# Performance work log

Measured on AMD Instinct MI355X. Metric: run time of the kernel, lower is better.

The kernel has to match this reference:

```python
import jax, jax.numpy as jnp
import numpy as np
import math

D_MODEL = 512
N_HEADS = 8
KSIZE = 3
SEQ = 2048
BATCH = 4


def setup_inputs() -> dict:
    key = jax.random.key(0)
    ks = jax.random.split(key, 12)
    f32 = jnp.float32
    scale_in = 1.0 / math.sqrt(D_MODEL)
    inp = {
        "query": jax.random.normal(ks[0], (SEQ, BATCH, D_MODEL), f32),
        "key": jax.random.normal(ks[1], (SEQ, BATCH, D_MODEL), f32),
        "value": jax.random.normal(ks[2], (SEQ, BATCH, D_MODEL), f32),
        # causal mask: 1 where attention allowed (lower triangular), 0 elsewhere
        "attn_mask": jnp.tril(jnp.ones((SEQ, SEQ), jnp.int32)),
        "conv1_w": jax.random.normal(ks[3], (D_MODEL, D_MODEL, KSIZE), f32) * scale_in,
        "conv1_b": jax.random.normal(ks[4], (D_MODEL,), f32) * 0.01,
        "conv2_w": jax.random.normal(ks[5], (D_MODEL, D_MODEL, KSIZE), f32) * scale_in,
        "conv2_b": jax.random.normal(ks[6], (D_MODEL,), f32) * 0.01,
        "lin1_w": jax.random.normal(ks[7], (D_MODEL, D_MODEL), f32) * scale_in,
        "lin1_b": jax.random.normal(ks[8], (D_MODEL,), f32) * 0.01,
        "lin2_w": jax.random.normal(ks[9], (D_MODEL, D_MODEL), f32) * scale_in,
        "lin2_b": jax.random.normal(ks[10], (D_MODEL,), f32) * 0.01,
    }
    return inp


def _causal_conv1d(x, w, b):
    # x: [B, S, C_in]; w: [C_out, C_in, K] (torch Conv1d layout); left-pad K-1 (causal)
    K = w.shape[-1]
    xc = jnp.transpose(x, (0, 2, 1))  # [B, C, S]
    y = jax.lax.conv_general_dilated(
        xc, w, window_strides=(1,), padding=[(K - 1, 0)],
        dimension_numbers=("NCH", "OIH", "NCH"))
    y = y + b[None, :, None]
    return jnp.transpose(y, (0, 2, 1))  # [B, S, C_out]


def reference(query, key, value, attn_mask,
              conv1_w, conv1_b, conv2_w, conv2_b,
              lin1_w, lin1_b, lin2_w, lin2_b):
    h, dk = N_HEADS, D_MODEL // N_HEADS
    S, B, D = query.shape
    q = jnp.transpose(query, (1, 0, 2))  # [B, S, D]
    k = jnp.transpose(key, (1, 0, 2))
    v = jnp.transpose(value, (1, 0, 2))

    q = _causal_conv1d(q, conv1_w, conv1_b).reshape(B, S, h, dk).transpose(0, 2, 1, 3)
    k = _causal_conv1d(k, conv2_w, conv2_b).reshape(B, S, h, dk).transpose(0, 2, 1, 3)
    v = (v @ lin1_w.T + lin1_b).reshape(B, S, h, dk).transpose(0, 2, 1, 3)

    scores = jnp.einsum("bhqd,bhkd->bhqk", q, k) / math.sqrt(dk)
    scores = jnp.where(attn_mask[None, None, :, :] == 0, jnp.float32(-1e9), scores)
    p_attn = jax.nn.softmax(scores, axis=-1)  # dropout p=0.0 (deterministic)
    x = jnp.einsum("bhqk,bhkd->bhqd", p_attn, v)
    x = x.transpose(0, 2, 1, 3).reshape(B, S, D)
    out = x @ lin2_w.T + lin2_b
    return jnp.transpose(out, (1, 0, 2))  # back to [S, B, D]
```

## Files before the change

kernel.cpp:

```cpp
#include <hip/hip_runtime.h>
#include <hip/hip_bf16.h>

#define S_LEN 2048
#define BATCH 4
#define DMODEL 512
#define NHEADS 8
#define DK 64
#define NELEM 4194304
#define WSLOT 786432

typedef __hip_bfloat16 bf16;
typedef unsigned short u16_t;
typedef __attribute__((ext_vector_type(8))) short bfx8;
typedef __attribute__((ext_vector_type(4))) short bfx4;
typedef __attribute__((ext_vector_type(4))) float fx4;

#define MFMA16(a, b, c) __builtin_amdgcn_mfma_f32_16x16x32_bf16(a, b, c, 0, 0, 0)

__device__ __forceinline__ float cvt(float x) { return x; }
__device__ __forceinline__ float cvt(bf16 x) { return __bfloat162float(x); }
__device__ __forceinline__ u16_t f2b(float x) { bf16 h = __float2bfloat16(x); return *(u16_t*)&h; }
__device__ __forceinline__ float b2f16(u16_t u) { bf16 h = *(bf16*)&u; return __bfloat162float(h); }

__global__ void sniff_kernel(const u16_t* __restrict__ q, int* __restrict__ flag) {
    const int lane = threadIdx.x & 63;
    int cnt = 0;
    for (int j = 0; j < 4; j++) {
        int e = (q[2 * (lane + 64 * j)] >> 7) & 0xFF;
        cnt += (int)__popcll(__ballot(e >= 100 && e <= 140));
    }
    if (lane == 0 && blockIdx.x == 0) *flag = (cnt >= 200) ? 1 : 0;
}

__global__ void cvt_in_kernel(const void* __restrict__ q, const void* __restrict__ k,
                              const void* __restrict__ v, u16_t* __restrict__ am,
                              const int* __restrict__ flag) {
    int gid = blockIdx.x * 256 + threadIdx.x;
    int e8 = gid * 8;
    int z = e8 >> 22;
    int off = e8 & (NELEM - 1);
    const void* src = (z == 0) ? q : (z == 1) ? k : v;
    u16_t* dst = am + (size_t)z * NELEM + off;
    if (*flag) {
        *(bfx8*)dst = *(const bfx8*)((const u16_t*)src + off);
    } else {
        const float* s = (const float*)src + off;
        fx4 a = *(const fx4*)s;
        fx4 b = *(const fx4*)(s + 4);
        u16_t tmp[8];
#pragma unroll
        for (int j = 0; j < 4; j++) { tmp[j] = f2b(a[j]); tmp[4 + j] = f2b(b[j]); }
        *(bfx8*)dst = *(const bfx8*)tmp;
    }
}

__global__ void cvt_w_kernel(const void* __restrict__ c1w, const void* __restrict__ c2w,
                             const void* __restrict__ l1w, const void* __restrict__ l2w,
                             const void* __restrict__ b0, const void* __restrict__ b1,
                             const void* __restrict__ b2, const void* __restrict__ b3,
                             u16_t* __restrict__ wt, u16_t* __restrict__ bb,
                             const int* __restrict__ flag) {
    const int isbf = *flag;
    if (blockIdx.x >= 3072) {
        int i = (blockIdx.x - 3072) * 256 + threadIdx.x;
        int p = i >> 9, o = i & 511;
        const void* b = (p == 0) ? b0 : (p == 1) ? b1 : (p == 2) ? b2 : b3;
        bb[i] = f2b(isbf ? cvt(((const bf16*)b)[o]) : ((const float*)b)[o]);
        return;
    }
    int gid = blockIdx.x * 256 + threadIdx.x;
    int e4 = gid * 4;
    int p = e4 / WSLOT;
    int r = e4 - p * WSLOT;
    int t = r >> 18;
    int rem = r & 262143;
    int o = rem >> 9, kk = rem & 511;
    const void* w = (p == 0) ? c1w : (p == 1) ? c2w : (p == 2) ? l1w : l2w;
    u16_t out[4];
#pragma unroll
    for (int j = 0; j < 4; j++) {
        float val;
        if (p < 2) {
            int idx = (o * DMODEL + kk + j) * 3 + t;
            val = isbf ? cvt(((const bf16*)w)[idx]) : ((const float*)w)[idx];
        } else {
            if (t == 2) {
                int idx = o * DMODEL + kk + j;
                val = isbf ? cvt(((const bf16*)w)[idx]) : ((const float*)w)[idx];
            } else val = 0.f;
        }
        out[j] = f2b(val);
    }
    *(bfx4*)(wt + e4) = *(const bfx4*)out;
}

template <int MODE>
__global__ __launch_bounds__(256) void uproj_kernel(
    const u16_t* __restrict__ X, const u16_t* __restrict__ Wt,
    const u16_t* __restrict__ Bb, u16_t* __restrict__ Y,
    void* __restrict__ dout, const int* __restrict__ flag) {
    constexpr int SMEM = (MODE == 0) ? 32832 : 23040;
    __shared__ __align__(16) u16_t smem[SMEM];
    const int tid = threadIdx.x;
    const int wave = tid >> 6, lane = tid & 63;
    const int l16 = lane & 15, quad = lane >> 4;
    const int mb_base = blockIdx.x * 256;
    const int nb_base = blockIdx.y * 64;
    const int z = blockIdx.z;
    const int isconv = (MODE == 0) && (z < 2);
    const u16_t* Xz = X + (size_t)((MODE == 0) ? z : 0) * NELEM;
    const u16_t* Wz = Wt + (size_t)((MODE == 0) ? z : 3) * WSLOT;
    const u16_t* Bz = Bb + ((MODE == 0) ? z : 3) * DMODEL;

    fx4 acc[4][4];
#pragma unroll
    for (int mb = 0; mb < 4; mb++)
#pragma unroll
        for (int nb = 0; nb < 4; nb++) acc[mb][nb] = (fx4){0.f, 0.f, 0.f, 0.f};

    if (isconv) {
        u16_t (*as_)[72] = (u16_t (*)[72])smem;
        u16_t (*ws_)[64][72] = (u16_t (*)[64][72])(smem + 19008);
        bfx8 pa[9], pw[6];
        {
            const int kc = 0;
#pragma unroll
            for (int j = 0; j < 9; j++) {
                int i = tid + 256 * j;
                if (i < 2112) {
                    int r = i >> 3, c8 = (i & 7) << 3;
                    int gm = mb_base - 8 + r;
                    if (gm >= 0) pa[j] = *(const bfx8*)(Xz + (size_t)gm * DMODEL + (kc << 6) + c8);
                    else { bfx8 zv; for (int jj = 0; jj < 8; jj++) zv[jj] = 0; pa[j] = zv; }
                }
            }
#pragma unroll
            for (int j = 0; j < 6; j++) {
                int i = tid + 256 * j;
                int t = i >> 9, rr = (i >> 3) & 63, c8 = (i & 7) << 3;
                pw[j] = *(const bfx8*)(Wz + (size_t)(t * DMODEL + nb_base + rr) * DMODEL + (kc << 6) + c8);
            }
        }
        for (int kc = 0; kc < 8; kc++) {
            __syncthreads();
#pragma unroll
            for (int j = 0; j < 9; j++) {
                int i = tid + 256 * j;
                if (i < 2112) { int r = i >> 3, c8 = (i & 7) << 3; *(bfx8*)&as_[r][c8] = pa[j]; }
            }
#pragma unroll
            for (int j = 0; j < 6; j++) {
                int i = tid + 256 * j;
                int t = i >> 9, rr = (i >> 3) & 63, c8 = (i & 7) << 3;
                *(bfx8*)&ws_[t][rr][c8] = pw[j];
            }
            __syncthreads();
            if (kc < 7) {
                const int kn = kc + 1;
#pragma unroll
                for (int j = 0; j < 9; j++) {
                    int i = tid + 256 * j;
                    if (i < 2112) {
                        int r = i >> 3, c8 = (i & 7) << 3;
                        int gm = mb_base - 8 + r;
                        if (gm >= 0) pa[j] = *(const bfx8*)(Xz + (size_t)gm * DMODEL + (kn << 6) + c8);
                        else { bfx8 zv; for (int jj = 0; jj < 8; jj++) zv[jj] = 0; pa[j] = zv; }
                    }
                }
#pragma unroll
                for (int j = 0; j < 6; j++) {
                    int i = tid + 256 * j;
                    int t = i >> 9, rr = (i >> 3) & 63, c8 = (i & 7) << 3;
                    pw[j] = *(const bfx8*)(Wz + (size_t)(t * DMODEL + nb_base + rr) * DMODEL + (kn << 6) + c8);
                }
            }
#pragma unroll
            for (int c = 0; c < 2; c++) {
#pragma unroll
                for (int t = 0; t < 3; t++) {
                    const int roff = 4 * t;
                    bfx8 av[4];
#pragma unroll
                    for (int mb = 0; mb < 4; mb++)
                        av[mb] = *(const bfx8*)&as_[wave * 64 + mb * 16 + l16 + roff][c * 32 + quad * 8];
#pragma unroll
                    for (int nb = 0; nb < 4; nb++) {
                        bfx8 bfr = *(const bfx8*)&ws_[t][nb * 16 + l16][c * 32 + quad * 8];
#pragma unroll
                        for (int mb = 0; mb < 4; mb++)
                            acc[mb][nb] = MFMA16(av[mb], bfr, acc[mb][nb]);
                    }
                }
            }
        }
    } else {
        u16_t (*as_)[72] = (u16_t (*)[72])smem;
        u16_t (*wsl)[72] = (u16_t (*)[72])(smem + ((MODE == 0) ? 19008 : 18432));
        const u16_t* Wlin = Wz + 2 * (size_t)DMODEL * DMODEL;
        bfx8 pa[8], pw[2];
        {
            const int kc = 0;
#pragma unroll
            for (int j = 0; j < 8; j++) {
                int i = tid + 256 * j;
                int r = i >> 3, c8 = (i & 7) << 3;
                pa[j] = *(const bfx8*)(Xz + (size_t)(mb_base + r) * DMODEL + (kc << 6) + c8);
            }
#pragma unroll
            for (int j = 0; j < 2; j++) {
                int i = tid + 256 * j;
                int rr = i >> 3, c8 = (i & 7) << 3;
                pw[j] = *(const bfx8*)(Wlin + (size_t)(nb_base + rr) * DMODEL + (kc << 6) + c8);
            }
        }
        for (int kc = 0; kc < 8; kc++) {
            __syncthreads();
#pragma unroll
            for (int j = 0; j < 8; j++) {
                int i = tid + 256 * j;
                int r = i >> 3, c8 = (i & 7) << 3;
                *(bfx8*)&as_[r][c8] = pa[j];
            }
#pragma unroll
            for (int j = 0; j < 2; j++) {
                int i = tid + 256 * j;
                int rr = i >> 3, c8 = (i & 7) << 3;
                *(bfx8*)&wsl[rr][c8] = pw[j];
            }
            __syncthreads();
            if (kc < 7) {
                const int kn = kc + 1;
#pragma unroll
                for (int j = 0; j < 8; j++) {
                    int i = tid + 256 * j;
                    int r = i >> 3, c8 = (i & 7) << 3;
                    pa[j] = *(const bfx8*)(Xz + (size_t)(mb_base + r) * DMODEL + (kn << 6) + c8);
                }
#pragma unroll
                for (int j = 0; j < 2; j++) {
                    int i = tid + 256 * j;
                    int rr = i >> 3, c8 = (i & 7) << 3;
                    pw[j] = *(const bfx8*)(Wlin + (size_t)(nb_base + rr) * DMODEL + (kn << 6) + c8);
                }
            }
#pragma unroll
            for (int c = 0; c < 2; c++) {
                bfx8 av[4];
#pragma unroll
                for (int mb = 0; mb < 4; mb++)
                    av[mb] = *(const bfx8*)&as_[wave * 64 + mb * 16 + l16][c * 32 + quad * 8];
#pragma unroll
                for (int nb = 0; nb < 4; nb++) {
                    bfx8 bfr = *(const bfx8*)&wsl[nb * 16 + l16][c * 32 + quad * 8];
#pragma unroll
                    for (int mb = 0; mb < 4; mb++)
                        acc[mb][nb] = MFMA16(av[mb], bfr, acc[mb][nb]);
                }
            }
        }
    }

    const int isbf = *flag;
#pragma unroll
    for (int mb = 0; mb < 4; mb++)
#pragma unroll
        for (int nb = 0; nb < 4; nb++)
#pragma unroll
            for (int r = 0; r < 4; r++) {
                int m = mb_base + wave * 64 + mb * 16 + quad * 4 + r;
                int o = nb_base + nb * 16 + l16;
                float val = acc[mb][nb][r] + b2f16(Bz[o]);
                if (MODE == 0) {
                    int s = m >> 2, b2 = m & 3, h2 = o >> 6, d2 = o & 63;
                    size_t idx = (z == 2)
                        ? (((size_t)(b2 * NHEADS + h2) * DK + d2) * S_LEN + s)
                        : (((size_t)(b2 * NHEADS + h2) * S_LEN + s) * DK + d2);
                    Y[(size_t)z * NELEM + idx] = f2b(val);
                } else {
                    if (isbf) ((bf16*)dout)[(size_t)m * DMODEL + o] = __float2bfloat16(val);
                    else      ((float*)dout)[(size_t)m * DMODEL + o] = val;
                }
            }
}

__global__ __launch_bounds__(256) void mattn_kernel(
    const u16_t* __restrict__ Qp, const u16_t* __restrict__ Kp,
    const u16_t* __restrict__ VpT, u16_t* __restrict__ Out) {
    __shared__ __align__(16) u16_t ks_[64][72];
    __shared__ __align__(16) u16_t vs[64][72];
    const int tid = threadIdx.x, wave = tid >> 6, lane = tid & 63;
    const int l16 = lane & 15, quad = lane >> 4;
    const int flat = (int)blockIdx.y * 16 + (int)blockIdx.x;
    const int swz = (flat & 7) * 64 + (flat >> 3);
    const int bh = swz >> 4;
    const int bx = swz & 15;
    const int bb2 = bh >> 3, hh2 = bh & 7;
    const int qts[2] = {bx, 31 - bx};

    const int r0 = tid >> 3, c8 = (tid & 7) << 3;
    const int pc0 = (c8 & 35) | ((c8 & 16) >> 2) | ((c8 & 12) << 1);
    const int c84 = c8 + 4;
    const int pc1 = (c84 & 35) | ((c84 & 16) >> 2) | ((c84 & 12) << 1);

    bfx8 qa[2][2];
#pragma unroll
    for (int j = 0; j < 2; j++) {
        const u16_t* qptr = Qp + (size_t)(bh * S_LEN + (qts[j] << 6) + wave * 16 + l16) * DK + quad * 8;
        qa[j][0] = *(const bfx8*)qptr;
        qa[j][1] = *(const bfx8*)(qptr + 32);
    }
    fx4 o_[2][4];
    float psum[2] = {0.f, 0.f};
#pragma unroll
    for (int j = 0; j < 2; j++)
#pragma unroll
        for (int nf = 0; nf < 4; nf++) o_[j][nf] = (fx4){0.f, 0.f, 0.f, 0.f};

    bfx8 kf0 = *(const bfx8*)(Kp + (size_t)(bh * S_LEN + r0) * DK + c8);
    bfx8 kf1 = *(const bfx8*)(Kp + (size_t)(bh * S_LEN + r0 + 32) * DK + c8);
    bfx8 vf0 = *(const bfx8*)(VpT + (size_t)(bh * DK + r0) * S_LEN + c8);
    bfx8 vf1 = *(const bfx8*)(VpT + (size_t)(bh * DK + r0 + 32) * S_LEN + c8);

    const int qg0 = (qts[0] << 6) + wave * 16 + l16;
    const int qg1 = (qts[1] << 6) + wave * 16 + l16;

    const int ktmax = qts[1];
    for (int kt = 0; kt <= ktmax; kt++) {
        const int kbase = kt << 6;
        __syncthreads();
        *(bfx8*)&ks_[r0][c8] = kf0;
        *(bfx8*)&ks_[r0 + 32][c8] = kf1;
        {
            bfx4 a0 = {vf0[0], vf0[1], vf0[2], vf0[3]};
            bfx4 a1 = {vf0[4], vf0[5], vf0[6], vf0[7]};
            bfx4 b0 = {vf1[0], vf1[1], vf1[2], vf1[3]};
            bfx4 b1 = {vf1[4], vf1[5], vf1[6], vf1[7]};
            *(bfx4*)&vs[r0][pc0] = a0;
            *(bfx4*)&vs[r0][pc1] = a1;
            *(bfx4*)&vs[r0 + 32][pc0] = b0;
            *(bfx4*)&vs[r0 + 32][pc1] = b1;
        }
        __syncthreads();
        if (kt < ktmax) {
            const int nb = (kt + 1) << 6;
            kf0 = *(const bfx8*)(Kp + (size_t)(bh * S_LEN + nb + r0) * DK + c8);
            kf1 = *(const bfx8*)(Kp + (size_t)(bh * S_LEN + nb + r0 + 32) * DK + c8);
            vf0 = *(const bfx8*)(VpT + (size_t)(bh * DK + r0) * S_LEN + nb + c8);
            vf1 = *(const bfx8*)(VpT + (size_t)(bh * DK + r0 + 32) * S_LEN + nb + c8);
        }

        bfx8 ak[2][4];
#pragma unroll
        for (int c = 0; c < 2; c++)
#pragma unroll
            for (int nf = 0; nf < 4; nf++)
                ak[c][nf] = *(const bfx8*)&ks_[nf * 16 + l16][c * 32 + quad * 8];

        bfx8 pb[2][2];
#pragma unroll
        for (int j = 0; j < 2; j++) {
            if (kt > qts[j]) continue;
            fx4 s[4];
#pragma unroll
            for (int nf = 0; nf < 4; nf++) {
                fx4 a = (fx4){0.f, 0.f, 0.f, 0.f};
                a = MFMA16(ak[0][nf], qa[j][0], a);
                a = MFMA16(ak[1][nf], qa[j][1], a);
                s[nf] = a;
            }
            const bool last = (kt == qts[j]);
            const int qgj = (j == 0) ? qg0 : qg1;
            float tsum = 0.f;
#pragma unroll
            for (int nf = 0; nf < 4; nf++) {
                float pr[4];
#pragma unroll
                for (int r = 0; r < 4; r++) {
                    float p = __builtin_amdgcn_exp2f(fmaf(s[nf][r], 0.18033688f, -17.3123405f));
                    if (last) {
                        int kg = kbase + nf * 16 + quad * 4 + r;
                        if (kg > qgj) p = 0.f;
                    }
                    pr[r] = p;
                    pb[j][nf >> 1][(nf & 1) * 4 + r] = (short)f2b(p);
                }
                tsum += (pr[0] + pr[1]) + (pr[2] + pr[3]);
            }
            psum[j] += tsum;
        }

        bfx8 av[2][4];
#pragma unroll
        for (int c = 0; c < 2; c++)
#pragma unroll
            for (int nf = 0; nf < 4; nf++)
                av[c][nf] = *(const bfx8*)&vs[nf * 16 + l16][c * 32 + quad * 8];
#pragma unroll
        for (int j = 0; j < 2; j++) {
            if (kt > qts[j]) continue;
#pragma unroll
            for (int nf = 0; nf < 4; nf++) {
                o_[j][nf] = MFMA16(av[0][nf], pb[j][0], o_[j][nf]);
                o_[j][nf] = MFMA16(av[1][nf], pb[j][1], o_[j][nf]);
            }
        }
    }

    float l_[2];
#pragma unroll
    for (int j = 0; j < 2; j++) {
        float v = psum[j];
        v += __shfl_xor(v, 16);
        v += __shfl_xor(v, 32);
        l_[j] = fmaxf(v, 1e-30f);
    }

#pragma unroll
    for (int j = 0; j < 2; j++) {
        const float inv = 1.0f / l_[j];
        const int qg = (j == 0) ? qg0 : qg1;
#pragma unroll
        for (int nf = 0; nf < 4; nf++) {
            bfx4 ov;
#pragma unroll
            for (int r = 0; r < 4; r++) ov[r] = (short)f2b(o_[j][nf][r] * inv);
            *(bfx4*)(Out + (size_t)(qg * 4 + bb2) * DMODEL + hh2 * 64 + nf * 16 + quad * 4) = ov;
        }
    }
}

extern "C" void kernel_launch(void* const* d_in, const int* in_sizes, int n_in,
                              void* d_out, int out_size, void* d_ws, size_t ws_size,
                              hipStream_t stream) {
    const void* q   = d_in[0];
    const void* k   = d_in[1];
    const void* v   = d_in[2];
    const void* c1w = d_in[4];
    const void* c1b = d_in[5];
    const void* c2w = d_in[6];
    const void* c2b = d_in[7];
    const void* l1w = d_in[8];
    const void* l1b = d_in[9];
    const void* l2w = d_in[10];
    const void* l2b = d_in[11];

    const size_t TEN = (size_t)NELEM * 2;
    char* base = (char*)d_ws;
    int* flag  = (int*)base;
    u16_t* am  = (u16_t*)(base + 512);
    u16_t* qp  = am + 3 * (size_t)NELEM;
    u16_t* kp  = am + 4 * (size_t)NELEM;
    u16_t* vpt = am + 5 * (size_t)NELEM;
    u16_t* wt  = (u16_t*)(base + 512 + 6 * TEN);
    u16_t* bb  = wt + 4 * (size_t)WSLOT;
    u16_t* ctx2 = am;

    sniff_kernel<<<dim3(1), dim3(64), 0, stream>>>((const u16_t*)q, flag);
    cvt_in_kernel<<<dim3(6144), dim3(256), 0, stream>>>(q, k, v, am, flag);
    cvt_w_kernel<<<dim3(3080), dim3(256), 0, stream>>>(c1w, c2w, l1w, l2w,
                                                       c1b, c2b, l1b, l2b, wt, bb, flag);
    uproj_kernel<0><<<dim3(32, 8, 3), dim3(256), 0, stream>>>(am, wt, bb, qp, nullptr, flag);
    mattn_kernel<<<dim3(16, 32), dim3(256), 0, stream>>>(qp, kp, vpt, ctx2);
    uproj_kernel<1><<<dim3(32, 8, 1), dim3(256), 0, stream>>>(ctx2, wt, bb, nullptr, d_out, flag);
}
```

Before: 224.9 us.

## Split paired causal q-tiles into one q-tile per block, doubling grid size

The attention kernel previously paired q-tile bx with 31-bx in each block, so every block did the same amount of causal work and shared its K/V tile loads between two query tiles. Now each block handles a single 64-row query tile, and the grid doubles to 1024 blocks with an 8-way swizzle. The aim is lower register pressure and more blocks in flight. In exchange, blocks now carry unequal amounts of work and K/V tiles are loaded from global memory about twice as often in total.

```diff
diff --git a/kernel.cpp b/kernel.cpp
--- a/kernel.cpp
+++ b/kernel.cpp
@@ -290,42 +290,36 @@
     __shared__ __align__(16) u16_t vs[64][72];
     const int tid = threadIdx.x, wave = tid >> 6, lane = tid & 63;
     const int l16 = lane & 15, quad = lane >> 4;
-    const int flat = (int)blockIdx.y * 16 + (int)blockIdx.x;
-    const int swz = (flat & 7) * 64 + (flat >> 3);
-    const int bh = swz >> 4;
-    const int bx = swz & 15;
+    const int flat = (int)blockIdx.y * 32 + (int)blockIdx.x;
+    const int swz = (flat & 7) * 128 + (flat >> 3);
+    const int bh = swz >> 5;
+    const int qt = swz & 31;
     const int bb2 = bh >> 3, hh2 = bh & 7;
-    const int qts[2] = {bx, 31 - bx};
 
     const int r0 = tid >> 3, c8 = (tid & 7) << 3;
     const int pc0 = (c8 & 35) | ((c8 & 16) >> 2) | ((c8 & 12) << 1);
     const int c84 = c8 + 4;
     const int pc1 = (c84 & 35) | ((c84 & 16) >> 2) | ((c84 & 12) << 1);
 
-    bfx8 qa[2][2];
-#pragma unroll
-    for (int j = 0; j < 2; j++) {
-        const u16_t* qptr = Qp + (size_t)(bh * S_LEN + (qts[j] << 6) + wave * 16 + l16) * DK + quad * 8;
-        qa[j][0] = *(const bfx8*)qptr;
-        qa[j][1] = *(const bfx8*)(qptr + 32);
-    }
-    fx4 o_[2][4];
-    float psum[2] = {0.f, 0.f};
-#pragma unroll
-    for (int j = 0; j < 2; j++)
-#pragma unroll
-        for (int nf = 0; nf < 4; nf++) o_[j][nf] = (fx4){0.f, 0.f, 0.f, 0.f};
+    bfx8 qa0, qa1;
+    {
+        const u16_t* qptr = Qp + (size_t)(bh * S_LEN + (qt << 6) + wave * 16 + l16) * DK + quad * 8;
+        qa0 = *(const bfx8*)qptr;
+        qa1 = *(const bfx8*)(qptr + 32);
+    }
+    fx4 o_[4];
+    float psum = 0.f;
+#pragma unroll
+    for (int nf = 0; nf < 4; nf++) o_[nf] = (fx4){0.f, 0.f, 0.f, 0.f};
 
     bfx8 kf0 = *(const bfx8*)(Kp + (size_t)(bh * S_LEN + r0) * DK + c8);
     bfx8 kf1 = *(const bfx8*)(Kp + (size_t)(bh * S_LEN + r0 + 32) * DK + c8);
     bfx8 vf0 = *(const bfx8*)(VpT + (size_t)(bh * DK + r0) * S_LEN + c8);
     bfx8 vf1 = *(const bfx8*)(VpT + (size_t)(bh * DK + r0 + 32) * S_LEN + c8);
 
-    const int qg0 = (qts[0] << 6) + wave * 16 + l16;
-    const int qg1 = (qts[1] << 6) + wave * 16 + l16;
-
-    const int ktmax = qts[1];
-    for (int kt = 0; kt <= ktmax; kt++) {
+    const int qg = (qt << 6) + wave * 16 + l16;
+
+    for (int kt = 0; kt <= qt; kt++) {
         const int kbase = kt << 6;
         __syncthreads();
         *(bfx8*)&ks_[r0][c8] = kf0;
@@ -341,7 +335,7 @@
             *(bfx4*)&vs[r0 + 32][pc1] = b1;
         }
         __syncthreads();
-        if (kt < ktmax) {
+        if (kt < qt) {
             const int nb = (kt + 1) << 6;
             kf0 = *(const bfx8*)(Kp + (size_t)(bh * S_LEN + nb + r0) * DK + c8);
             kf1 = *(const bfx8*)(Kp + (size_t)(bh * S_LEN + nb + r0 + 32) * DK + c8);
@@ -349,83 +343,56 @@
             vf1 = *(const bfx8*)(VpT + (size_t)(bh * DK + r0 + 32) * S_LEN + nb + c8);
         }
 
-        bfx8 ak[2][4];
-#pragma unroll
-        for (int c = 0; c < 2; c++)
-#pragma unroll
-            for (int nf = 0; nf < 4; nf++)
-                ak[c][nf] = *(const bfx8*)&ks_[nf * 16 + l16][c * 32 + quad * 8];
-
-        bfx8 pb[2][2];
-#pragma unroll
-        for (int j = 0; j < 2; j++) {
-            if (kt > qts[j]) continue;
-            fx4 s[4];
-#pragma unroll
-            for (int nf = 0; nf < 4; nf++) {
-                fx4 a = (fx4){0.f, 0.f, 0.f, 0.f};
-                a = MFMA16(ak[0][nf], qa[j][0], a);
-                a = MFMA16(ak[1][nf], qa[j][1], a);
-                s[nf] = a;
-            }
-            const bool last = (kt == qts[j]);
-            const int qgj = (j == 0) ? qg0 : qg1;
-            float tsum = 0.f;
-#pragma unroll
-            for (int nf = 0; nf < 4; nf++) {
-                float pr[4];
-#pragma unroll
-                for (int r = 0; r < 4; r++) {
-                    float p = __builtin_amdgcn_exp2f(fmaf(s[nf][r], 0.18033688f, -17.3123405f));
-                    if (last) {
-                        int kg = kbase + nf * 16 + quad * 4 + r;
-                        if (kg > qgj) p = 0.f;
-                    }
-                    pr[r] = p;
-                    pb[j][nf >> 1][(nf & 1) * 4 + r] = (short)f2b(p);
-                }
-                tsum += (pr[0] + pr[1]) + (pr[2] + pr[3]);
-            }
-            psum[j] += tsum;
-        }
-
-        bfx8 av[2][4];
-#pragma unroll
-        for (int c = 0; c < 2; c++)
-#pragma unroll
-            for (int nf = 0; nf < 4; nf++)
-                av[c][nf] = *(const bfx8*)&vs[nf * 16 + l16][c * 32 + quad * 8];
-#pragma unroll
-        for (int j = 0; j < 2; j++) {
-            if (kt > qts[j]) continue;
-#pragma unroll
-            for (int nf = 0; nf < 4; nf++) {
-                o_[j][nf] = MFMA16(av[0][nf], pb[j][0], o_[j][nf]);
-                o_[j][nf] = MFMA16(av[1][nf], pb[j][1], o_[j][nf]);
-            }
-        }
-    }
-
-    float l_[2];
-#pragma unroll
-    for (int j = 0; j < 2; j++) {
-        float v = psum[j];
-        v += __shfl_xor(v, 16);
-        v += __shfl_xor(v, 32);
-        l_[j] = fmaxf(v, 1e-30f);
-    }
-
-#pragma unroll
-    for (int j = 0; j < 2; j++) {
-        const float inv = 1.0f / l_[j];
-        const int qg = (j == 0) ? qg0 : qg1;
+        fx4 s[4];
 #pragma unroll
         for (int nf = 0; nf < 4; nf++) {
-            bfx4 ov;
-#pragma unroll
-            for (int r = 0; r < 4; r++) ov[r] = (short)f2b(o_[j][nf][r] * inv);
-            *(bfx4*)(Out + (size_t)(qg * 4 + bb2) * DMODEL + hh2 * 64 + nf * 16 + quad * 4) = ov;
-        }
+            bfx8 k0 = *(const bfx8*)&ks_[nf * 16 + l16][quad * 8];
+            bfx8 k1 = *(const bfx8*)&ks_[nf * 16 + l16][32 + quad * 8];
+            fx4 a = (fx4){0.f, 0.f, 0.f, 0.f};
+            a = MFMA16(k0, qa0, a);
+            a = MFMA16(k1, qa1, a);
+            s[nf] = a;
+        }
+        const bool last = (kt == qt);
+        bfx8 pb[2];
+        float tsum = 0.f;
+#pragma unroll
+        for (int nf = 0; nf < 4; nf++) {
+            float pr[4];
+#pragma unroll
+            for (int r = 0; r < 4; r++) {
+                float p = __builtin_amdgcn_exp2f(fmaf(s[nf][r], 0.18033688f, -17.3123405f));
+                if (last) {
+                    int kg = kbase + nf * 16 + quad * 4 + r;
+                    if (kg > qg) p = 0.f;
+                }
+                pr[r] = p;
+                pb[nf >> 1][(nf & 1) * 4 + r] = (short)f2b(p);
+            }
+            tsum += (pr[0] + pr[1]) + (pr[2] + pr[3]);
+        }
+        psum += tsum;
+
+#pragma unroll
+        for (int nf = 0; nf < 4; nf++) {
+            bfx8 v0 = *(const bfx8*)&vs[nf * 16 + l16][quad * 8];
+            bfx8 v1 = *(const bfx8*)&vs[nf * 16 + l16][32 + quad * 8];
+            o_[nf] = MFMA16(v0, pb[0], o_[nf]);
+            o_[nf] = MFMA16(v1, pb[1], o_[nf]);
+        }
+    }
+
+    float v = psum;
+    v += __shfl_xor(v, 16);
+    v += __shfl_xor(v, 32);
+    const float inv = 1.0f / fmaxf(v, 1e-30f);
+
+#pragma unroll
+    for (int nf = 0; nf < 4; nf++) {
+        bfx4 ov;
+#pragma unroll
+        for (int r = 0; r < 4; r++) ov[r] = (short)f2b(o_[nf][r] * inv);
+        *(bfx4*)(Out + (size_t)(qg * 4 + bb2) * DMODEL + hh2 * 64 + nf * 16 + quad * 4) = ov;
     }
 }
 
@@ -460,6 +427,6 @@
     cvt_w_kernel<<<dim3(3080), dim3(256), 0, stream>>>(c1w, c2w, l1w, l2w,
                                                        c1b, c2b, l1b, l2b, wt, bb, flag);
     uproj_kernel<0><<<dim3(32, 8, 3), dim3(256), 0, stream>>>(am, wt, bb, qp, nullptr, flag);
-    mattn_kernel<<<dim3(16, 32), dim3(256), 0, stream>>>(qp, kp, vpt, ctx2);
+    mattn_kernel<<<dim3(32, 32), dim3(256), 0, stream>>>(qp, kp, vpt, ctx2);
     uproj_kernel<1><<<dim3(32, 8, 1), dim3(256), 0, stream>>>(ctx2, wt, bb, nullptr, d_out, flag);
 }
```

New measurement: 236.4 us. +5.1%, slower.

## Load K/V MFMA fragments directly from global memory, dropping LDS staging

Applied to the files above, without the earlier changes.

Removes the shared-memory tiles for K and V, along with the two __syncthreads per key tile and the register prefetch. Each wave now reads its MFMA operand fragments straight from global memory, relying on L1/L2 to serve the four waves that read the same data. V fragments are built from two 4-element loads, matching the permuted layout the old LDS path produced. This saves LDS traffic and barriers, but costs four times the global load requests and exposes load latency that the old prefetch used to hide.

```diff
diff --git a/kernel.cpp b/kernel.cpp
--- a/kernel.cpp
+++ b/kernel.cpp
@@ -286,8 +286,6 @@
 __global__ __launch_bounds__(256) void mattn_kernel(
     const u16_t* __restrict__ Qp, const u16_t* __restrict__ Kp,
     const u16_t* __restrict__ VpT, u16_t* __restrict__ Out) {
-    __shared__ __align__(16) u16_t ks_[64][72];
-    __shared__ __align__(16) u16_t vs[64][72];
     const int tid = threadIdx.x, wave = tid >> 6, lane = tid & 63;
     const int l16 = lane & 15, quad = lane >> 4;
     const int flat = (int)blockIdx.y * 16 + (int)blockIdx.x;
@@ -297,10 +295,8 @@
     const int bb2 = bh >> 3, hh2 = bh & 7;
     const int qts[2] = {bx, 31 - bx};
 
-    const int r0 = tid >> 3, c8 = (tid & 7) << 3;
-    const int pc0 = (c8 & 35) | ((c8 & 16) >> 2) | ((c8 & 12) << 1);
-    const int c84 = c8 + 4;
-    const int pc1 = (c84 & 35) | ((c84 & 16) >> 2) | ((c84 & 12) << 1);
+    const u16_t* kfp = Kp + (size_t)(bh * S_LEN + l16) * DK + quad * 8;
+    const u16_t* vfp = VpT + (size_t)(bh * DK + l16) * S_LEN + quad * 4;
 
     bfx8 qa[2][2];
 #pragma unroll
@@ -316,45 +312,33 @@
 #pragma unroll
         for (int nf = 0; nf < 4; nf++) o_[j][nf] = (fx4){0.f, 0.f, 0.f, 0.f};
 
-    bfx8 kf0 = *(const bfx8*)(Kp + (size_t)(bh * S_LEN + r0) * DK + c8);
-    bfx8 kf1 = *(const bfx8*)(Kp + (size_t)(bh * S_LEN + r0 + 32) * DK + c8);
-    bfx8 vf0 = *(const bfx8*)(VpT + (size_t)(bh * DK + r0) * S_LEN + c8);
-    bfx8 vf1 = *(const bfx8*)(VpT + (size_t)(bh * DK + r0 + 32) * S_LEN + c8);
-
     const int qg0 = (qts[0] << 6) + wave * 16 + l16;
     const int qg1 = (qts[1] << 6) + wave * 16 + l16;
 
     const int ktmax = qts[1];
     for (int kt = 0; kt <= ktmax; kt++) {
         const int kbase = kt << 6;
-        __syncthreads();
-        *(bfx8*)&ks_[r0][c8] = kf0;
-        *(bfx8*)&ks_[r0 + 32][c8] = kf1;
-        {
-            bfx4 a0 = {vf0[0], vf0[1], vf0[2], vf0[3]};
-            bfx4 a1 = {vf0[4], vf0[5], vf0[6], vf0[7]};
-            bfx4 b0 = {vf1[0], vf1[1], vf1[2], vf1[3]};
-            bfx4 b1 = {vf1[4], vf1[5], vf1[6], vf1[7]};
-            *(bfx4*)&vs[r0][pc0] = a0;
-            *(bfx4*)&vs[r0][pc1] = a1;
-            *(bfx4*)&vs[r0 + 32][pc0] = b0;
-            *(bfx4*)&vs[r0 + 32][pc1] = b1;
-        }
-        __syncthreads();
-        if (kt < ktmax) {
-            const int nb = (kt + 1) << 6;
-            kf0 = *(const bfx8*)(Kp + (size_t)(bh * S_LEN + nb + r0) * DK + c8);
-            kf1 = *(const bfx8*)(Kp + (size_t)(bh * S_LEN + nb + r0 + 32) * DK + c8);
-            vf0 = *(const bfx8*)(VpT + (size_t)(bh * DK + r0) * S_LEN + nb + c8);
-            vf1 = *(const bfx8*)(VpT + (size_t)(bh * DK + r0 + 32) * S_LEN + nb + c8);
-        }
 
         bfx8 ak[2][4];
 #pragma unroll
         for (int c = 0; c < 2; c++)
 #pragma unroll
             for (int nf = 0; nf < 4; nf++)
-                ak[c][nf] = *(const bfx8*)&ks_[nf * 16 + l16][c * 32 + quad * 8];
+                ak[c][nf] = *(const bfx8*)(kfp + (size_t)(kbase + nf * 16) * DK + c * 32);
+
+        bfx8 av[2][4];
+#pragma unroll
+        for (int c = 0; c < 2; c++)
+#pragma unroll
+            for (int nf = 0; nf < 4; nf++) {
+                const u16_t* vp = vfp + (size_t)(nf * 16) * S_LEN + kbase + c * 32;
+                bfx4 lo = *(const bfx4*)vp;
+                bfx4 hi = *(const bfx4*)(vp + 16);
+                bfx8 t;
+                t[0] = lo[0]; t[1] = lo[1]; t[2] = lo[2]; t[3] = lo[3];
+                t[4] = hi[0]; t[5] = hi[1]; t[6] = hi[2]; t[7] = hi[3];
+                av[c][nf] = t;
+            }
 
         bfx8 pb[2][2];
 #pragma unroll
@@ -389,12 +373,6 @@
             psum[j] += tsum;
         }
 
-        bfx8 av[2][4];
-#pragma unroll
-        for (int c = 0; c < 2; c++)
-#pragma unroll
-            for (int nf = 0; nf < 4; nf++)
-                av[c][nf] = *(const bfx8*)&vs[nf * 16 + l16][c * 32 + quad * 8];
 #pragma unroll
         for (int j = 0; j < 2; j++) {
             if (kt > qts[j]) continue;
```

Result: slower. 354.3 us (+57.6%).
